# Optimization experiments

Measured on AMD Instinct MI355X. Metric: run time of the kernel, lower is better.

Reference implementation:

```python
import jax, jax.numpy as jnp
import numpy as np

N_USER, N_ENTITY, N_RELATION = 100000, 2000000, 64
BATCH, N_NEIGHBOR, DIM = 65536, 8, 16
L2_WEIGHT = 1e-4


def setup_inputs() -> dict:
    key = jax.random.key(0)
    ks = jax.random.split(key, 10)
    inp = {
        # parameters: torch.rand(..)*2-1 -> uniform(-1,1)
        "user_emb": jax.random.uniform(ks[0], (N_USER, DIM), jnp.float32, -1.0, 1.0),
        "entity_emb": jax.random.uniform(ks[1], (N_ENTITY, DIM), jnp.float32, -1.0, 1.0),
        "relation_emb": jax.random.uniform(ks[2], (N_RELATION, DIM), jnp.float32, -1.0, 1.0),
        "agg_W": jax.random.normal(ks[3], (DIM, DIM), jnp.float32) * (1.0 / np.sqrt(DIM)),
        "agg_b": jnp.zeros((DIM,), jnp.float32),
        "labels": jnp.round(jax.random.uniform(ks[4], (BATCH,), jnp.float32)),
        "user_indices": jax.random.randint(ks[5], (BATCH,), 0, N_USER, jnp.int32),
        "item_indices": jax.random.randint(ks[6], (BATCH,), 0, N_ENTITY, jnp.int32),
        "adj_entity": jax.random.randint(ks[7], (N_ENTITY, N_NEIGHBOR), 0, N_ENTITY, jnp.int32),
        "adj_relation": jax.random.randint(ks[8], (N_ENTITY, N_NEIGHBOR), 0, N_RELATION, jnp.int32),
    }
    return inp


def reference(user_emb, entity_emb, relation_emb, agg_W, agg_b, labels,
              user_indices, item_indices, adj_entity, adj_relation):
    # --- gathers (1-hop, n_iter=1) ---
    u = user_emb[user_indices]                      # [B, D]
    self_vec = entity_emb[item_indices]             # [B, D]
    nbr_e = adj_entity[item_indices]                # [B, K]
    nbr_r = adj_relation[item_indices]              # [B, K]
    nbr_vecs = entity_emb[nbr_e]                    # [B, K, D]
    rel_vecs = relation_emb[nbr_r]                  # [B, K, D]

    # --- SumAggregator: user-relation attention over neighbors ---
    scores = jnp.mean(u[:, None, :] * rel_vecs, axis=-1)     # [B, K]
    attn = jax.nn.softmax(scores, axis=-1)                   # [B, K]
    nbr_agg = jnp.einsum('bk,bkd->bd', attn, nbr_vecs)       # [B, D]

    # Linear(dim,dim) + tanh (act on last hop)
    item_emb = jnp.tanh((self_vec + nbr_agg) @ agg_W.T + agg_b)  # [B, D]

    # --- score + BCE loss + L2 ---
    logits = jnp.sum(u * item_emb, axis=1)                   # [B]
    # -y*log(sigmoid(x)) - (1-y)*log(1-sigmoid(x)), stable form
    base_loss = jnp.mean(-labels * jax.nn.log_sigmoid(logits)
                         - (1.0 - labels) * jax.nn.log_sigmoid(-logits))
    l2 = 0.5 * (jnp.sum(user_emb ** 2) + jnp.sum(entity_emb ** 2)
                + jnp.sum(relation_emb ** 2))
    return base_loss + L2_WEIGHT * l2
```

## Files before the change

kernel.cpp:

```cpp
#include <hip/hip_runtime.h>
#include <math.h>

#define BATCH     65536
#define NNBR      8
#define DIM       16
#define HALF_L2W  5.0e-5f

#define FUSED_GRID   4096
#define FUSED_BLOCK  256

__global__ void __launch_bounds__(FUSED_BLOCK)
fused_kernel(const float* __restrict__ ue,
             const float* __restrict__ ee,
             const float* __restrict__ re,
             const float* __restrict__ W,
             const float* __restrict__ bias,
             const float* __restrict__ labels,
             const int*   __restrict__ uidx,
             const int*   __restrict__ iidx,
             const int*   __restrict__ adjE,
             const int*   __restrict__ adjR,
             int n_u4, int n_e4, int n_r4,
             float* __restrict__ ws) {
    __shared__ float sW[DIM * DIM];
    __shared__ float sb[DIM];
    if (threadIdx.x < DIM * DIM) sW[threadIdx.x] = W[threadIdx.x];
    if (threadIdx.x < DIM)       sb[threadIdx.x] = bias[threadIdx.x];
    __syncthreads();

    const int lane = threadIdx.x & 15;
    const int grp  = threadIdx.x >> 4;
    const int row  = blockIdx.x * 16 + grp;

    const int ui = uidx[row];
    const int it = iidx[row];

    const float u  = ue[ui * DIM + lane];
    const float sv = ee[it * DIM + lane];

    int ne[NNBR], nr[NNBR];
    #pragma unroll
    for (int k = 0; k < NNBR; ++k) {
        ne[k] = adjE[it * NNBR + k];
        nr[k] = adjR[it * NNBR + k];
    }

    float nv[NNBR];
    float sc[NNBR];
    #pragma unroll
    for (int k = 0; k < NNBR; ++k) {
        const float rv = re[nr[k] * DIM + lane];
        nv[k] = ee[ne[k] * DIM + lane];
        float s = u * rv;
        #pragma unroll
        for (int o = 8; o > 0; o >>= 1) s += __shfl_xor(s, o, 16);
        sc[k] = s * (1.0f / 16.0f);
    }

    float m = sc[0];
    #pragma unroll
    for (int k = 1; k < NNBR; ++k) m = fmaxf(m, sc[k]);
    float den = 0.0f;
    float e[NNBR];
    #pragma unroll
    for (int k = 0; k < NNBR; ++k) { e[k] = __expf(sc[k] - m); den += e[k]; }
    const float inv = 1.0f / den;

    float agg = 0.0f;
    #pragma unroll
    for (int k = 0; k < NNBR; ++k) agg += e[k] * nv[k];
    agg *= inv;

    const float x = sv + agg;

    float acc = sb[lane];
    #pragma unroll
    for (int j = 0; j < DIM; ++j) {
        const float xj = __shfl(x, j, 16);
        acc += sW[lane * DIM + j] * xj;
    }
    const float item = tanhf(acc);

    float lg = u * item;
    #pragma unroll
    for (int o = 8; o > 0; o >>= 1) lg += __shfl_xor(lg, o, 16);

    float bce = 0.0f;
    if (lane == 0) {
        const float y = labels[row];
        bce = fmaxf(lg, 0.0f) - lg * y + log1pf(__expf(-fabsf(lg)));
    }

    const float4* ue4 = (const float4*)ue;
    const float4* ee4 = (const float4*)ee;
    const float4* re4 = (const float4*)re;

    float l2 = 0.0f;
    {
        const int tid    = blockIdx.x * FUSED_BLOCK + threadIdx.x;
        const int stride = FUSED_GRID * FUSED_BLOCK;
        for (int i = tid; i < n_e4; i += stride) {
            float4 v = ee4[i];
            l2 += v.x * v.x + v.y * v.y + v.z * v.z + v.w * v.w;
        }
        for (int i = tid; i < n_u4; i += stride) {
            float4 v = ue4[i];
            l2 += v.x * v.x + v.y * v.y + v.z * v.z + v.w * v.w;
        }
        for (int i = tid; i < n_r4; i += stride) {
            float4 v = re4[i];
            l2 += v.x * v.x + v.y * v.y + v.z * v.z + v.w * v.w;
        }
    }

    #pragma unroll
    for (int o = 32; o > 0; o >>= 1) {
        bce += __shfl_down(bce, o);
        l2  += __shfl_down(l2, o);
    }

    __shared__ float sred[8];
    const int wid = threadIdx.x >> 6;
    if ((threadIdx.x & 63) == 0) { sred[wid] = l2; sred[4 + wid] = bce; }
    __syncthreads();
    if (threadIdx.x == 0) {
        ws[2 * blockIdx.x]     = sred[0] + sred[1] + sred[2] + sred[3];
        ws[2 * blockIdx.x + 1] = sred[4] + sred[5] + sred[6] + sred[7];
    }
}

__global__ void __launch_bounds__(256)
finalize_kernel(const float* __restrict__ ws, float* __restrict__ out) {
    float l2 = 0.0f, bce = 0.0f;
    for (int i = threadIdx.x; i < FUSED_GRID; i += 256) {
        l2  += ws[2 * i];
        bce += ws[2 * i + 1];
    }
    #pragma unroll
    for (int o = 32; o > 0; o >>= 1) {
        l2  += __shfl_down(l2, o);
        bce += __shfl_down(bce, o);
    }
    __shared__ float sred[8];
    const int wid = threadIdx.x >> 6;
    if ((threadIdx.x & 63) == 0) { sred[wid] = l2; sred[4 + wid] = bce; }
    __syncthreads();
    if (threadIdx.x == 0) {
        const float l2t  = sred[0] + sred[1] + sred[2] + sred[3];
        const float bcet = sred[4] + sred[5] + sred[6] + sred[7];
        out[0] = bcet * (1.0f / (float)BATCH) + HALF_L2W * l2t;
    }
}

extern "C" void kernel_launch(void* const* d_in, const int* in_sizes, int n_in,
                              void* d_out, int out_size, void* d_ws, size_t ws_size,
                              hipStream_t stream) {
    const float* user_emb     = (const float*)d_in[0];
    const float* entity_emb   = (const float*)d_in[1];
    const float* relation_emb = (const float*)d_in[2];
    const float* agg_W        = (const float*)d_in[3];
    const float* agg_b        = (const float*)d_in[4];
    const float* labels       = (const float*)d_in[5];
    const int*   user_indices = (const int*)d_in[6];
    const int*   item_indices = (const int*)d_in[7];
    const int*   adj_entity   = (const int*)d_in[8];
    const int*   adj_relation = (const int*)d_in[9];

    float* ws  = (float*)d_ws;
    float* out = (float*)d_out;

    const int n_u4 = in_sizes[0] / 4;
    const int n_e4 = in_sizes[1] / 4;
    const int n_r4 = in_sizes[2] / 4;

    fused_kernel<<<FUSED_GRID, FUSED_BLOCK, 0, stream>>>(
        user_emb, entity_emb, relation_emb, agg_W, agg_b, labels,
        user_indices, item_indices, adj_entity, adj_relation,
        n_u4, n_e4, n_r4, ws);

    finalize_kernel<<<1, 256, 0, stream>>>(ws, out);
}
```

Before: 46.16 us.

## Use 4-lane float4 rows, fewer blocks, and compile-time unrolled L2 sweep

```diff
diff --git a/kernel.cpp b/kernel.cpp
--- a/kernel.cpp
+++ b/kernel.cpp
@@ -6,111 +6,128 @@
 #define DIM       16
 #define HALF_L2W  5.0e-5f
 
-#define FUSED_GRID   4096
-#define FUSED_BLOCK  256
+#define GRID      1024
+#define BLOCK     256
+#define NTH       (GRID * BLOCK)
+#define ROWS_PB   64
 
-__global__ void __launch_bounds__(FUSED_BLOCK)
-fused_kernel(const float* __restrict__ ue,
-             const float* __restrict__ ee,
-             const float* __restrict__ re,
-             const float* __restrict__ W,
-             const float* __restrict__ bias,
-             const float* __restrict__ labels,
-             const int*   __restrict__ uidx,
-             const int*   __restrict__ iidx,
-             const int*   __restrict__ adjE,
-             const int*   __restrict__ adjR,
-             int n_u4, int n_e4, int n_r4,
+#define N_E4      8000000
+#define N_U4      400000
+#define N_R4      256
+
+#define E_ITERS   (N_E4 / NTH)
+#define E_TAIL    (N_E4 - E_ITERS * NTH)
+#define U_TAIL    (N_U4 - NTH)
+
+__device__ __forceinline__ float sq4(float4 v) {
+    return v.x * v.x + v.y * v.y + v.z * v.z + v.w * v.w;
+}
+
+__global__ void __launch_bounds__(BLOCK, 4)
+fused_kernel(const float4* __restrict__ ue4,
+             const float4* __restrict__ ee4,
+             const float4* __restrict__ re4,
+             const float*  __restrict__ W,
+             const float4* __restrict__ b4,
+             const float*  __restrict__ labels,
+             const int*    __restrict__ uidx,
+             const int*    __restrict__ iidx,
+             const int4*   __restrict__ adjE4,
+             const int4*   __restrict__ adjR4,
              float* __restrict__ ws) {
-    __shared__ float sW[DIM * DIM];
-    __shared__ float sb[DIM];
-    if (threadIdx.x < DIM * DIM) sW[threadIdx.x] = W[threadIdx.x];
-    if (threadIdx.x < DIM)       sb[threadIdx.x] = bias[threadIdx.x];
+    __shared__ float sWT[DIM * DIM];
+    __shared__ float4 sb4[DIM / 4];
+    if (threadIdx.x < DIM * DIM)
+        sWT[threadIdx.x] = W[(threadIdx.x & 15) * DIM + (threadIdx.x >> 4)];
+    if (threadIdx.x < DIM / 4) sb4[threadIdx.x] = b4[threadIdx.x];
     __syncthreads();
 
-    const int lane = threadIdx.x & 15;
-    const int grp  = threadIdx.x >> 4;
-    const int row  = blockIdx.x * 16 + grp;
+    const int lane4 = threadIdx.x & 3;
+    const int rgrp  = threadIdx.x >> 2;
+    const int row   = blockIdx.x * ROWS_PB + rgrp;
+    const int tid_g = blockIdx.x * BLOCK + threadIdx.x;
 
     const int ui = uidx[row];
     const int it = iidx[row];
+    const float4 u4  = ue4[ui * 4 + lane4];
+    const float4 sv4 = ee4[it * 4 + lane4];
+    const int4 a0 = adjE4[it * 2], a1 = adjE4[it * 2 + 1];
+    const int4 r0 = adjR4[it * 2], r1 = adjR4[it * 2 + 1];
 
-    const float u  = ue[ui * DIM + lane];
-    const float sv = ee[it * DIM + lane];
-
-    int ne[NNBR], nr[NNBR];
-    #pragma unroll
-    for (int k = 0; k < NNBR; ++k) {
-        ne[k] = adjE[it * NNBR + k];
-        nr[k] = adjR[it * NNBR + k];
+    float l2 = 0.0f;
+    {
+        const float4* p = ee4 + tid_g;
+        #pragma unroll
+        for (int k = 0; k < E_ITERS; ++k) l2 += sq4(p[k * NTH]);
+        if (tid_g < E_TAIL) l2 += sq4(p[E_ITERS * NTH]);
+        l2 += sq4(ue4[tid_g]);
+        if (tid_g < U_TAIL) l2 += sq4(ue4[tid_g + NTH]);
+        if (tid_g < N_R4)   l2 += sq4(re4[tid_g]);
     }
 
-    float nv[NNBR];
+    const int ne[NNBR] = {a0.x, a0.y, a0.z, a0.w, a1.x, a1.y, a1.z, a1.w};
+    const int nr[NNBR] = {r0.x, r0.y, r0.z, r0.w, r1.x, r1.y, r1.z, r1.w};
+
+    float4 nv[NNBR];
     float sc[NNBR];
     #pragma unroll
     for (int k = 0; k < NNBR; ++k) {
-        const float rv = re[nr[k] * DIM + lane];
-        nv[k] = ee[ne[k] * DIM + lane];
-        float s = u * rv;
-        #pragma unroll
-        for (int o = 8; o > 0; o >>= 1) s += __shfl_xor(s, o, 16);
+        const float4 rv = re4[nr[k] * 4 + lane4];
+        nv[k] = ee4[ne[k] * 4 + lane4];
+        float s = u4.x * rv.x + u4.y * rv.y + u4.z * rv.z + u4.w * rv.w;
+        s += __shfl_xor(s, 1, 4);
+        s += __shfl_xor(s, 2, 4);
         sc[k] = s * (1.0f / 16.0f);
     }
 
     float m = sc[0];
     #pragma unroll
     for (int k = 1; k < NNBR; ++k) m = fmaxf(m, sc[k]);
-    float den = 0.0f;
-    float e[NNBR];
+    float e[NNBR], den = 0.0f;
     #pragma unroll
     for (int k = 0; k < NNBR; ++k) { e[k] = __expf(sc[k] - m); den += e[k]; }
     const float inv = 1.0f / den;
 
-    float agg = 0.0f;
+    float4 agg = make_float4(0.f, 0.f, 0.f, 0.f);
     #pragma unroll
-    for (int k = 0; k < NNBR; ++k) agg += e[k] * nv[k];
-    agg *= inv;
+    for (int k = 0; k < NNBR; ++k) {
+        agg.x += e[k] * nv[k].x; agg.y += e[k] * nv[k].y;
+        agg.z += e[k] * nv[k].z; agg.w += e[k] * nv[k].w;
+    }
 
-    const float x = sv + agg;
+    float4 x4;
+    x4.x = sv4.x + agg.x * inv; x4.y = sv4.y + agg.y * inv;
+    x4.z = sv4.z + agg.z * inv; x4.w = sv4.w + agg.w * inv;
 
-    float acc = sb[lane];
+    float xall[DIM];
+    #pragma unroll
+    for (int src = 0; src < 4; ++src) {
+        xall[4 * src + 0] = __shfl(x4.x, src, 4);
+        xall[4 * src + 1] = __shfl(x4.y, src, 4);
+        xall[4 * src + 2] = __shfl(x4.z, src, 4);
+        xall[4 * src + 3] = __shfl(x4.w, src, 4);
+    }
+
+    const float4* sWT4 = (const float4*)sWT;
+    float4 acc = sb4[lane4];
     #pragma unroll
     for (int j = 0; j < DIM; ++j) {
-        const float xj = __shfl(x, j, 16);
-        acc += sW[lane * DIM + j] * xj;
+        const float4 wv = sWT4[j * 4 + lane4];
+        acc.x += xall[j] * wv.x; acc.y += xall[j] * wv.y;
+        acc.z += xall[j] * wv.z; acc.w += xall[j] * wv.w;
     }
-    const float item = tanhf(acc);
+    float4 item;
+    item.x = tanhf(acc.x); item.y = tanhf(acc.y);
+    item.z = tanhf(acc.z); item.w = tanhf(acc.w);
 
-    float lg = u * item;
-    #pragma unroll
-    for (int o = 8; o > 0; o >>= 1) lg += __shfl_xor(lg, o, 16);
+    float lg = u4.x * item.x + u4.y * item.y + u4.z * item.z + u4.w * item.w;
+    lg += __shfl_xor(lg, 1, 4);
+    lg += __shfl_xor(lg, 2, 4);
 
     float bce = 0.0f;
-    if (lane == 0) {
+    if (lane4 == 0) {
         const float y = labels[row];
         bce = fmaxf(lg, 0.0f) - lg * y + log1pf(__expf(-fabsf(lg)));
-    }
-
-    const float4* ue4 = (const float4*)ue;
-    const float4* ee4 = (const float4*)ee;
-    const float4* re4 = (const float4*)re;
-
-    float l2 = 0.0f;
-    {
-        const int tid    = blockIdx.x * FUSED_BLOCK + threadIdx.x;
-        const int stride = FUSED_GRID * FUSED_BLOCK;
-        for (int i = tid; i < n_e4; i += stride) {
-            float4 v = ee4[i];
-            l2 += v.x * v.x + v.y * v.y + v.z * v.z + v.w * v.w;
-        }
-        for (int i = tid; i < n_u4; i += stride) {
-            float4 v = ue4[i];
-            l2 += v.x * v.x + v.y * v.y + v.z * v.z + v.w * v.w;
-        }
-        for (int i = tid; i < n_r4; i += stride) {
-            float4 v = re4[i];
-            l2 += v.x * v.x + v.y * v.y + v.z * v.z + v.w * v.w;
-        }
     }
 
     #pragma unroll
@@ -118,7 +135,6 @@
         bce += __shfl_down(bce, o);
         l2  += __shfl_down(l2, o);
     }
-
     __shared__ float sred[8];
     const int wid = threadIdx.x >> 6;
     if ((threadIdx.x & 63) == 0) { sred[wid] = l2; sred[4 + wid] = bce; }
@@ -132,7 +148,9 @@
 __global__ void __launch_bounds__(256)
 finalize_kernel(const float* __restrict__ ws, float* __restrict__ out) {
     float l2 = 0.0f, bce = 0.0f;
-    for (int i = threadIdx.x; i < FUSED_GRID; i += 256) {
+    #pragma unroll
+    for (int k = 0; k < GRID / 256; ++k) {
+        const int i = threadIdx.x + k * 256;
         l2  += ws[2 * i];
         bce += ws[2 * i + 1];
     }
@@ -169,14 +187,11 @@
     float* ws  = (float*)d_ws;
     float* out = (float*)d_out;
 
-    const int n_u4 = in_sizes[0] / 4;
-    const int n_e4 = in_sizes[1] / 4;
-    const int n_r4 = in_sizes[2] / 4;
-
-    fused_kernel<<<FUSED_GRID, FUSED_BLOCK, 0, stream>>>(
-        user_emb, entity_emb, relation_emb, agg_W, agg_b, labels,
-        user_indices, item_indices, adj_entity, adj_relation,
-        n_u4, n_e4, n_r4, ws);
+    fused_kernel<<<GRID, BLOCK, 0, stream>>>(
+        (const float4*)user_emb, (const float4*)entity_emb, (const float4*)relation_emb,
+        agg_W, (const float4*)agg_b, labels,
+        user_indices, item_indices,
+        (const int4*)adj_entity, (const int4*)adj_relation, ws);
 
     finalize_kernel<<<1, 256, 0, stream>>>(ws, out);
 }
```

Result: slower. 49.46 us (+7.1%).
